# Kernel optimization log

Measured on AMD Instinct MI355X. Metric: run time of the kernel, lower is better.

Reference implementation:

```python
import jax, jax.numpy as jnp
import numpy as np

CH = 256
CH_HALF = CH // 2
HEADS = 2          # heads_half = max(1, 4 // 2)
WIN_R = (16, 4)
WIN_A = (4, 16)
EPS = 1e-5


def _rel_index(Wh, Ww):
    # Precomputed relative-position index, identical to RelPosBias.__init__
    coords = np.stack(np.meshgrid(np.arange(Wh), np.arange(Ww), indexing='ij'))
    coords = coords.reshape(2, -1)                      # [2, N]
    rel = coords[:, :, None] - coords[:, None, :]       # [2, N, N]
    rel = rel.transpose(1, 2, 0).copy()
    rel[..., 0] += Wh - 1
    rel[..., 1] += Ww - 1
    rel[..., 0] *= 2 * Ww - 1
    return jnp.asarray(rel.sum(-1))                     # [N, N] int


def _layernorm(x, g, b):
    m = jnp.mean(x, axis=-1, keepdims=True)
    v = jnp.mean((x - m) ** 2, axis=-1, keepdims=True)
    return (x - m) * jax.lax.rsqrt(v + EPS) * g + b


def _window_attn(xw, Wqkv, Wp, bp, table, window):
    # xw: [Bn, N, C]
    Bn, N, C = xw.shape
    d = C // HEADS
    qkv = (xw @ Wqkv).reshape(Bn, N, 3, HEADS, d).transpose(2, 0, 3, 1, 4)
    q, k, v = qkv[0], qkv[1], qkv[2]                    # [Bn, h, N, d]
    attn = jnp.einsum('bhnd,bhmd->bhnm', q, k) * (d ** -0.5)
    idx = _rel_index(*window)                           # [N, N]
    bias = table[idx.reshape(-1)].reshape(N, N, HEADS).transpose(2, 0, 1)
    attn = jax.nn.softmax(attn + bias[None], axis=-1)
    out = jnp.einsum('bhnm,bhmd->bhnd', attn, v)
    out = out.transpose(0, 2, 1, 3).reshape(Bn, N, C)
    return out @ Wp + bp


def _branch(x, window, Wqkv, Wp, bp, table):
    # x: [B, H, W, C]; window partition -> attn -> residual -> reverse
    B, H, W, C = x.shape
    Wh, Ww = window
    xw = x.reshape(B, H // Wh, Wh, W // Ww, Ww, C)
    xw = xw.transpose(0, 1, 3, 2, 4, 5).reshape(-1, Wh * Ww, C)
    xw = xw + _window_attn(xw, Wqkv, Wp, bp, table, window)
    x = xw.reshape(B, H // Wh, W // Ww, Wh, Ww, C)
    x = x.transpose(0, 1, 3, 2, 4, 5).reshape(B, H, W, C)
    return x


def setup_inputs() -> dict:
    key = jax.random.key(0)
    ks = jax.random.split(key, 16)
    N_R = (2 * WIN_R[0] - 1) * (2 * WIN_R[1] - 1)
    N_A = (2 * WIN_A[0] - 1) * (2 * WIN_A[1] - 1)
    s = lambda fan: (2.0 / fan) ** 0.5
    return {
        'x': jax.random.normal(ks[0], (1, CH, 256, 256), jnp.float32),
        'norm1_g': jnp.ones((CH,), jnp.float32),
        'norm1_b': jnp.zeros((CH,), jnp.float32),
        'qkv_r': jax.random.normal(ks[1], (CH_HALF, 3 * CH_HALF), jnp.float32) * s(CH_HALF),
        'proj_r_w': jax.random.normal(ks[2], (CH_HALF, CH_HALF), jnp.float32) * s(CH_HALF),
        'proj_r_b': jnp.zeros((CH_HALF,), jnp.float32),
        'table_r': jax.random.normal(ks[3], (N_R, HEADS), jnp.float32) * 0.02,
        'qkv_a': jax.random.normal(ks[4], (CH_HALF, 3 * CH_HALF), jnp.float32) * s(CH_HALF),
        'proj_a_w': jax.random.normal(ks[5], (CH_HALF, CH_HALF), jnp.float32) * s(CH_HALF),
        'proj_a_b': jnp.zeros((CH_HALF,), jnp.float32),
        'table_a': jax.random.normal(ks[6], (N_A, HEADS), jnp.float32) * 0.02,
        'norm2_g': jnp.ones((CH,), jnp.float32),
        'norm2_b': jnp.zeros((CH,), jnp.float32),
        'mlp_w1': jax.random.normal(ks[7], (CH, 4 * CH), jnp.float32) * s(CH),
        'mlp_b1': jnp.zeros((4 * CH,), jnp.float32),
        'mlp_w2': jax.random.normal(ks[8], (4 * CH, CH), jnp.float32) * s(4 * CH),
        'mlp_b2': jnp.zeros((CH,), jnp.float32),
    }


def reference(x, norm1_g, norm1_b, qkv_r, proj_r_w, proj_r_b, table_r,
              qkv_a, proj_a_w, proj_a_b, table_a, norm2_g, norm2_b,
              mlp_w1, mlp_b1, mlp_w2, mlp_b2):
    # x: [B, C, H, W]; H, W divisible by 16 -> pad is a no-op
    x = x.transpose(0, 2, 3, 1)                          # [B, H, W, C]
    idt = x
    xn = _layernorm(x, norm1_g, norm1_b)
    out_r = _branch(xn[..., :CH_HALF], WIN_R, qkv_r, proj_r_w, proj_r_b, table_r)
    out_a = _branch(xn[..., CH_HALF:], WIN_A, qkv_a, proj_a_w, proj_a_b, table_a)
    x = idt + jnp.concatenate([out_r, out_a], axis=-1)
    h = _layernorm(x, norm2_g, norm2_b)
    h = jax.nn.gelu(h @ mlp_w1 + mlp_b1, approximate=False) @ mlp_w2 + mlp_b2
    x = x + h
    return x.transpose(0, 3, 1, 2)                       # back to [B, C, H, W]
```

## Files before the change

kernel.cpp:

```cpp
#include <hip/hip_runtime.h>
#include <stdint.h>

typedef unsigned short ushort_t;
typedef __attribute__((ext_vector_type(8))) short short8;
typedef __attribute__((ext_vector_type(4))) float floatx4;
typedef __attribute__((ext_vector_type(16))) float floatx16;
typedef __attribute__((ext_vector_type(4))) unsigned int u32x4;

__device__ __forceinline__ float bf2f(ushort_t u) {
    union { unsigned int i; float f; } v; v.i = ((unsigned int)u) << 16; return v.f;
}
__device__ __forceinline__ ushort_t f2bf(float f) {
    union { float ff; unsigned int i; } v; v.ff = f;
    unsigned int x = v.i;
    return (ushort_t)((x + 0x7fffu + ((x >> 16) & 1u)) >> 16);
}
__device__ __forceinline__ float gelu_f(float v) {
    float u = v * (0.7978845608f + 0.0356774081f * v * v);
    float e = __expf(2.f * u);
    float th = 1.f - 2.f / (e + 1.f);
    return 0.5f * v * (1.f + th);
}
#define LDS_ROUNDTRIP_FENCE() __asm__ volatile("s_waitcnt lgkmcnt(0)" ::: "memory")

__global__ __launch_bounds__(256) void prep_k(
    const float* __restrict__ x, const float* __restrict__ n1g, const float* __restrict__ n1b,
    ushort_t* __restrict__ xn,
    const float* __restrict__ qkv_r, ushort_t* __restrict__ wqkvT_r,
    const float* __restrict__ qkv_a, ushort_t* __restrict__ wqkvT_a,
    const float* __restrict__ pr_w,  ushort_t* __restrict__ wpT_r,
    const float* __restrict__ pa_w,  ushort_t* __restrict__ wpT_a,
    const float* __restrict__ w1,    ushort_t* __restrict__ w1p,
    const float* __restrict__ w2,    ushort_t* __restrict__ w2p)
{
    __shared__ __align__(16) char pshm[33792];
    const int t = threadIdx.x;
    int b = blockIdx.x;
    if (b < 1024) {
        ushort_t* tile = (ushort_t*)pshm;
        const int p0 = b * 64;
        {
            const int pg = t & 15, cb = t >> 4;
            for (int it = 0; it < 16; ++it) {
                int c = cb + 16 * it;
                floatx4 v = *(const floatx4*)(x + (size_t)c * 65536 + p0 + pg * 4);
                #pragma unroll
                for (int k = 0; k < 4; ++k) tile[(pg * 4 + k) * 264 + c] = f2bf(v[k]);
            }
        }
        __syncthreads();
        const int pix = t >> 2, part = t & 3;
        float vals[64];
        float s = 0.f, ss = 0.f;
        #pragma unroll
        for (int k = 0; k < 64; ++k) {
            float v = bf2f(tile[pix * 264 + part * 64 + k]);
            vals[k] = v; s += v; ss += v * v;
        }
        s  += __shfl_xor(s, 1);  s  += __shfl_xor(s, 2);
        ss += __shfl_xor(ss, 1); ss += __shfl_xor(ss, 2);
        float mean = s * (1.f / 256.f);
        float rstd = rsqrtf(ss * (1.f / 256.f) - mean * mean + 1e-5f);
        size_t obase = (size_t)(p0 + pix) * 256 + part * 64;
        #pragma unroll
        for (int k8 = 0; k8 < 8; ++k8) {
            alignas(16) ushort_t o8[8];
            #pragma unroll
            for (int k = 0; k < 8; ++k) {
                int c = part * 64 + k8 * 8 + k;
                o8[k] = f2bf((vals[k8 * 8 + k] - mean) * rstd * n1g[c] + n1b[c]);
            }
            *(u32x4*)(xn + obase + k8 * 8) = *(const u32x4*)o8;
        }
        return;
    }
    b -= 1024;
    if (b < 512) {
        const float* src; ushort_t* dst; int R, C, bi;
        if (b < 192)      { src = qkv_r; dst = wqkvT_r; R = 128; C = 384; bi = b;       }
        else if (b < 384) { src = qkv_a; dst = wqkvT_a; R = 128; C = 384; bi = b - 192; }
        else if (b < 448) { src = pr_w;  dst = wpT_r;   R = 128; C = 128; bi = b - 384; }
        else              { src = pa_w;  dst = wpT_a;   R = 128; C = 128; bi = b - 448; }
        int nbx = C / 16;
        int c0 = (bi % nbx) * 16, r0 = (bi / nbx) * 16;
        float* ts = (float*)pshm;
        int tx = t & 15, ty = t >> 4;
        ts[ty * 17 + tx] = src[(size_t)(r0 + ty) * C + (c0 + tx)];
        __syncthreads();
        dst[(size_t)(c0 + ty) * R + (r0 + tx)] = f2bf(ts[tx * 17 + ty]);
        return;
    }
    b -= 512;
    float* s = (float*)pshm;
    if (b < 64) {
        const int ch = b & 15, k0 = (b >> 4) * 64;
        {
            int nn = t & 63, kr = t >> 6;
            for (int j = 0; j < 16; ++j) {
                int kk = j * 4 + kr;
                s[kk * 65 + nn] = w1[(size_t)(k0 + kk) * 1024 + ch * 64 + nn];
            }
        }
        __syncthreads();
        {
            int kk = t & 63, nr = t >> 6;
            for (int j = 0; j < 16; ++j) {
                int n2 = j * 4 + nr;
                w1p[(size_t)ch * 16896 + n2 * 264 + k0 + kk] = f2bf(s[kk * 65 + n2]);
            }
        }
        return;
    }
    b -= 64;
    {
        const int ch = b & 15, n0 = (b >> 4) * 64;
        {
            int nn = t & 63, kr = t >> 6;
            for (int j = 0; j < 16; ++j) {
                int kk = j * 4 + kr;
                s[kk * 65 + nn] = w2[(size_t)(ch * 64 + kk) * 256 + n0 + nn];
            }
        }
        __syncthreads();
        {
            int kk = t & 63, nr = t >> 6;
            for (int j = 0; j < 16; ++j) {
                int n2 = j * 4 + nr;
                w2p[(size_t)ch * 18432 + (n0 + n2) * 72 + kk] = f2bf(s[kk * 65 + n2]);
            }
        }
    }
}

__global__ __launch_bounds__(256, 2) void attn_k(
    const ushort_t* __restrict__ xn,
    const ushort_t* __restrict__ wqkvT_r, const ushort_t* __restrict__ wpT_r,
    const float* __restrict__ bp_r, const float* __restrict__ table_r,
    const ushort_t* __restrict__ wqkvT_a, const ushort_t* __restrict__ wpT_a,
    const float* __restrict__ bp_a, const float* __restrict__ table_a,
    ushort_t* __restrict__ bout)
{
    __shared__ __align__(16) char smem_raw[71680];
    ushort_t* xw_s = (ushort_t*)smem_raw;
    ushort_t* q_s  = (ushort_t*)(smem_raw + 17408);
    ushort_t* k_s  = (ushort_t*)(smem_raw + 35840);
    ushort_t* v_s  = (ushort_t*)(smem_raw + 53248);

    const int br  = blockIdx.y;
    const int wid = blockIdx.x;
    const int t = threadIdx.x;
    const int wv = t >> 6, lane = t & 63, l15 = lane & 15, quad = lane >> 4;

    const int WwLog = br ? 4 : 2;
    const int WhLog = br ? 2 : 4;
    const int nWxLog = 8 - WwLog;
    const int wx = wid & ((1 << nWxLog) - 1);
    const int wy = wid >> nWxLog;
    const int chOff = br ? 128 : 0;
    const int WwM1 = (1 << WwLog) - 1, WhM1 = (1 << WhLog) - 1;
    const int biasMul = 2 * (1 << WwLog) - 1;
    const ushort_t* wqkvT = br ? wqkvT_a : wqkvT_r;
    const ushort_t* wpT   = br ? wpT_a   : wpT_r;
    const float* bp    = br ? bp_a    : bp_r;
    const float* table = br ? table_a : table_r;

    auto tok2p = [&](int n) -> int {
        int i = n >> WwLog, j = n & WwM1;
        return ((wy << WhLog) + i) * 256 + (wx << WwLog) + j;
    };

    {
        int tok = t >> 2, seg = t & 3;
        const ushort_t* src = xn + (size_t)tok2p(tok) * 256 + chOff + seg * 32;
        ushort_t* dst = xw_s + tok * 136 + seg * 32;
        *(u32x4*)(dst)      = *(const u32x4*)(src);
        *(u32x4*)(dst + 8)  = *(const u32x4*)(src + 8);
        *(u32x4*)(dst + 16) = *(const u32x4*)(src + 16);
        *(u32x4*)(dst + 24) = *(const u32x4*)(src + 24);
    }
    __syncthreads();

    {
        short8 afrag[4];
        #pragma unroll
        for (int kt = 0; kt < 4; ++kt)
            afrag[kt] = *(const short8*)(xw_s + (16 * wv + l15) * 136 + kt * 32 + quad * 8);
        for (int nt = 0; nt < 24; ++nt) {
            floatx4 acc = {0.f, 0.f, 0.f, 0.f};
            const ushort_t* wb = wqkvT + (size_t)(nt * 16 + l15) * 128 + quad * 8;
            #pragma unroll
            for (int kt = 0; kt < 4; ++kt)
                acc = __builtin_amdgcn_mfma_f32_16x16x32_bf16(afrag[kt],
                        *(const short8*)(wb + kt * 32), acc, 0, 0, 0);
            int ncol = nt * 16 + l15;
            #pragma unroll
            for (int r = 0; r < 4; ++r) {
                int row = 16 * wv + quad * 4 + r;
                ushort_t val = f2bf(acc[r]);
                if (ncol < 128)      q_s[row * 136 + ncol] = val;
                else if (ncol < 256) k_s[row * 136 + (ncol - 128)] = val;
                else                 v_s[(ncol - 256) * 72 + row] = val;
            }
        }
    }
    __syncthreads();

    float pvals[2][4][4];
    #pragma unroll
    for (int head = 0; head < 2; ++head) {
        floatx4 sacc[4];
        #pragma unroll
        for (int nt = 0; nt < 4; ++nt) sacc[nt] = floatx4{0.f, 0.f, 0.f, 0.f};
        #pragma unroll
        for (int kt = 0; kt < 2; ++kt) {
            short8 aq = *(const short8*)(q_s + (16 * wv + l15) * 136 + head * 64 + kt * 32 + quad * 8);
            #pragma unroll
            for (int nt = 0; nt < 4; ++nt) {
                short8 bk = *(const short8*)(k_s + (nt * 16 + l15) * 136 + head * 64 + kt * 32 + quad * 8);
                sacc[nt] = __builtin_amdgcn_mfma_f32_16x16x32_bf16(aq, bk, sacc[nt], 0, 0, 0);
            }
        }
        #pragma unroll
        for (int r = 0; r < 4; ++r) {
            int qrow = 16 * wv + quad * 4 + r;
            int iq = qrow >> WwLog, jq = qrow & WwM1;
            float v[4], mx = -1e30f;
            #pragma unroll
            for (int nt = 0; nt < 4; ++nt) {
                int kcol = nt * 16 + l15;
                int ik = kcol >> WwLog, jk = kcol & WwM1;
                int idx = (iq - ik + WhM1) * biasMul + (jq - jk + WwM1);
                v[nt] = sacc[nt][r] * 0.125f + table[idx * 2 + head];
                mx = fmaxf(mx, v[nt]);
            }
            mx = fmaxf(mx, __shfl_xor(mx, 1)); mx = fmaxf(mx, __shfl_xor(mx, 2));
            mx = fmaxf(mx, __shfl_xor(mx, 4)); mx = fmaxf(mx, __shfl_xor(mx, 8));
            float e[4], sm = 0.f;
            #pragma unroll
            for (int nt = 0; nt < 4; ++nt) { e[nt] = __expf(v[nt] - mx); sm += e[nt]; }
            sm += __shfl_xor(sm, 1); sm += __shfl_xor(sm, 2);
            sm += __shfl_xor(sm, 4); sm += __shfl_xor(sm, 8);
            float inv = 1.f / sm;
            #pragma unroll
            for (int nt = 0; nt < 4; ++nt) pvals[head][nt][r] = e[nt] * inv;
        }
    }
    __syncthreads();

    {
        ushort_t* p_s = q_s;
        #pragma unroll
        for (int head = 0; head < 2; ++head)
            #pragma unroll
            for (int nt = 0; nt < 4; ++nt)
                #pragma unroll
                for (int r = 0; r < 4; ++r) {
                    int row = 16 * wv + quad * 4 + r;
                    p_s[(head * 64 + row) * 72 + nt * 16 + l15] = f2bf(pvals[head][nt][r]);
                }
    }
    LDS_ROUNDTRIP_FENCE();
    {
        const ushort_t* p_s = q_s;
        ushort_t* o_s = k_s;
        #pragma unroll
        for (int head = 0; head < 2; ++head) {
            short8 ap[2];
            #pragma unroll
            for (int kt = 0; kt < 2; ++kt)
                ap[kt] = *(const short8*)(p_s + (head * 64 + 16 * wv + l15) * 72 + kt * 32 + quad * 8);
            #pragma unroll
            for (int nt = 0; nt < 4; ++nt) {
                floatx4 acc = {0.f, 0.f, 0.f, 0.f};
                #pragma unroll
                for (int kt = 0; kt < 2; ++kt) {
                    short8 bv = *(const short8*)(v_s + (head * 64 + nt * 16 + l15) * 72 + kt * 32 + quad * 8);
                    acc = __builtin_amdgcn_mfma_f32_16x16x32_bf16(ap[kt], bv, acc, 0, 0, 0);
                }
                #pragma unroll
                for (int r = 0; r < 4; ++r)
                    o_s[(16 * wv + quad * 4 + r) * 136 + head * 64 + nt * 16 + l15] = f2bf(acc[r]);
            }
        }
    }
    __syncthreads();

    {
        const ushort_t* o_s = k_s;
        short8 ao[4];
        #pragma unroll
        for (int kt = 0; kt < 4; ++kt)
            ao[kt] = *(const short8*)(o_s + (16 * wv + l15) * 136 + kt * 32 + quad * 8);
        #pragma unroll
        for (int nt = 0; nt < 8; ++nt) {
            floatx4 acc = {0.f, 0.f, 0.f, 0.f};
            const ushort_t* wb = wpT + (size_t)(nt * 16 + l15) * 128 + quad * 8;
            #pragma unroll
            for (int kt = 0; kt < 4; ++kt)
                acc = __builtin_amdgcn_mfma_f32_16x16x32_bf16(ao[kt],
                        *(const short8*)(wb + kt * 32), acc, 0, 0, 0);
            int col = nt * 16 + l15;
            float bpv = bp[col];
            #pragma unroll
            for (int r = 0; r < 4; ++r) {
                int row = 16 * wv + quad * 4 + r;
                float res = acc[r] + bpv + bf2f(xw_s[row * 136 + col]);
                bout[(size_t)tok2p(row) * 256 + chOff + col] = f2bf(res);
            }
        }
    }
}

__global__ __launch_bounds__(256, 2) void mlp_k(
    const float* __restrict__ x,
    const ushort_t* __restrict__ bout,
    const float* __restrict__ g2, const float* __restrict__ b2,
    const ushort_t* __restrict__ w1p, const float* __restrict__ b1,
    const ushort_t* __restrict__ w2p, const float* __restrict__ bm2,
    float* __restrict__ out)
{
    __shared__ __align__(16) char smem_raw[79872];
    ushort_t* x2_s = (ushort_t*)smem_raw;
    ushort_t* wbuf = (ushort_t*)(smem_raw + 33792);
    ushort_t* hbuf = (ushort_t*)(smem_raw + 70656);
    ushort_t* xn_s = wbuf;
    ushort_t* ot_s = (ushort_t*)smem_raw;

    const int t = threadIdx.x;
    const int p0 = blockIdx.x * 64;
    const int wv = t >> 6, lane = t & 63, l31 = lane & 31, half = lane >> 5;

    {
        const int pg = t & 15, cb = t >> 4;
        for (int it = 0; it < 16; ++it) {
            int c = cb + 16 * it;
            floatx4 v = *(const floatx4*)(x + (size_t)c * 65536 + p0 + pg * 4);
            #pragma unroll
            for (int k = 0; k < 4; ++k) x2_s[(pg * 4 + k) * 264 + c] = f2bf(v[k]);
        }
    }
    __syncthreads();
    {
        const int row = t >> 2, part = t & 3;
        float vals[64];
        float s = 0.f, ss = 0.f;
        const ushort_t* bpr = bout + (size_t)(p0 + row) * 256 + part * 64;
        ushort_t* xpr = x2_s + row * 264 + part * 64;
        #pragma unroll
        for (int k8 = 0; k8 < 8; ++k8) {
            u32x4 bv = *(const u32x4*)(bpr + k8 * 8);
            u32x4 xv = *(const u32x4*)(xpr + k8 * 8);
            const ushort_t* pb = (const ushort_t*)&bv;
            const ushort_t* px = (const ushort_t*)&xv;
            #pragma unroll
            for (int k = 0; k < 8; ++k) {
                float v = bf2f(px[k]) + bf2f(pb[k]);
                vals[k8 * 8 + k] = v; s += v; ss += v * v;
            }
        }
        s  += __shfl_xor(s, 1);  s  += __shfl_xor(s, 2);
        ss += __shfl_xor(ss, 1); ss += __shfl_xor(ss, 2);
        float mean = s * (1.f / 256.f);
        float rstd = rsqrtf(ss * (1.f / 256.f) - mean * mean + 1e-5f);
        const float* g2p = g2 + part * 64;
        const float* b2p = b2 + part * 64;
        ushort_t* npr = xn_s + row * 264 + part * 64;
        #pragma unroll
        for (int k8 = 0; k8 < 8; ++k8) {
            alignas(16) ushort_t o8[8], n8[8];
            #pragma unroll
            for (int k = 0; k < 8; ++k) {
                float v = vals[k8 * 8 + k];
                o8[k] = f2bf(v);
                n8[k] = f2bf((v - mean) * rstd * g2p[k8 * 8 + k] + b2p[k8 * 8 + k]);
            }
            *(u32x4*)(xpr + k8 * 8) = *(const u32x4*)o8;
            *(u32x4*)(npr + k8 * 8) = *(const u32x4*)n8;
        }
    }
    __syncthreads();

    const int g1m = wv & 1, g1n = wv >> 1;
    const int g2m = wv & 1;
    const int g2nb = 128 * (wv >> 1);

    short8 afrag[16];
    #pragma unroll
    for (int ks = 0; ks < 16; ++ks)
        afrag[ks] = *(const short8*)(xn_s + (32 * g1m + l31) * 264 + ks * 16 + half * 8);

    u32x4* wb16 = (u32x4*)wbuf;
    u32x4 w1reg[9], w2reg[9];
    {
        const u32x4* s1 = (const u32x4*)w1p;
        #pragma unroll
        for (int j = 0; j < 8; ++j) w1reg[j] = s1[j * 256 + t];
        if (t < 64) w1reg[8] = s1[2048 + t];
    }
    __syncthreads();
    {
        #pragma unroll
        for (int j = 0; j < 8; ++j) wb16[j * 256 + t] = w1reg[j];
        if (t < 64) wb16[2048 + t] = w1reg[8];
    }
    __syncthreads();

    floatx16 oacc[4];
    #pragma unroll
    for (int nt = 0; nt < 4; ++nt)
        #pragma unroll
        for (int i = 0; i < 16; ++i) oacc[nt][i] = 0.f;

    for (int ch = 0; ch < 16; ++ch) {
        {
            const u32x4* s2 = (const u32x4*)(w2p + (size_t)ch * 18432);
            #pragma unroll
            for (int j = 0; j < 9; ++j) w2reg[j] = s2[j * 256 + t];
        }
        floatx16 ha, hb;
        #pragma unroll
        for (int i = 0; i < 16; ++i) { ha[i] = 0.f; hb[i] = 0.f; }
        #pragma unroll
        for (int ks = 0; ks < 16; ks += 2) {
            short8 bf0 = *(const short8*)(wbuf + (32 * g1n + l31) * 264 + ks * 16 + half * 8);
            short8 bf1 = *(const short8*)(wbuf + (32 * g1n + l31) * 264 + ks * 16 + 16 + half * 8);
            ha = __builtin_amdgcn_mfma_f32_32x32x16_bf16(afrag[ks], bf0, ha, 0, 0, 0);
            hb = __builtin_amdgcn_mfma_f32_32x32x16_bf16(afrag[ks + 1], bf1, hb, 0, 0, 0);
        }
        {
            float bb = b1[ch * 64 + 32 * g1n + l31];
            #pragma unroll
            for (int r = 0; r < 16; ++r) {
                int row = 32 * g1m + (r & 3) + 8 * (r >> 2) + 4 * half;
                float v = gelu_f(ha[r] + hb[r] + bb);
                hbuf[row * 72 + 32 * g1n + l31] = f2bf(v);
            }
        }
        __syncthreads();
        {
            #pragma unroll
            for (int j = 0; j < 9; ++j) wb16[j * 256 + t] = w2reg[j];
        }
        __syncthreads();
        if (ch < 15) {
            const u32x4* s1 = (const u32x4*)(w1p + (size_t)(ch + 1) * 16896);
            #pragma unroll
            for (int j = 0; j < 8; ++j) w1reg[j] = s1[j * 256 + t];
            if (t < 64) w1reg[8] = s1[2048 + t];
        }
        #pragma unroll
        for (int ks = 0; ks < 4; ++ks) {
            short8 haf = *(const short8*)(hbuf + (32 * g2m + l31) * 72 + ks * 16 + half * 8);
            #pragma unroll
            for (int nt = 0; nt < 4; ++nt) {
                short8 bfr = *(const short8*)(wbuf + (g2nb + 32 * nt + l31) * 72 + ks * 16 + half * 8);
                oacc[nt] = __builtin_amdgcn_mfma_f32_32x32x16_bf16(haf, bfr, oacc[nt], 0, 0, 0);
            }
        }
        __syncthreads();
        if (ch < 15) {
            #pragma unroll
            for (int j = 0; j < 8; ++j) wb16[j * 256 + t] = w1reg[j];
            if (t < 64) wb16[2048 + t] = w1reg[8];
        }
        __syncthreads();
    }

    #pragma unroll
    for (int nt = 0; nt < 4; ++nt) {
        int col = g2nb + 32 * nt + l31;
        float bb = bm2[col];
        #pragma unroll
        for (int r = 0; r < 16; ++r) {
            int row = 32 * g2m + (r & 3) + 8 * (r >> 2) + 4 * half;
            oacc[nt][r] += bb + bf2f(x2_s[row * 264 + col]);
        }
    }
    __syncthreads();
    #pragma unroll
    for (int nt = 0; nt < 4; ++nt) {
        int col = g2nb + 32 * nt + l31;
        #pragma unroll
        for (int r = 0; r < 16; ++r) {
            int row = 32 * g2m + (r & 3) + 8 * (r >> 2) + 4 * half;
            ot_s[col * 72 + row] = f2bf(oacc[nt][r]);
        }
    }
    __syncthreads();
    {
        for (int it = 0; it < 64; ++it) {
            int c = it * 4 + wv;
            out[(size_t)c * 65536 + p0 + lane] = bf2f(ot_s[c * 72 + lane]);
        }
    }
}

extern "C" void kernel_launch(void* const* d_in, const int* in_sizes, int n_in,
                              void* d_out, int out_size, void* d_ws, size_t ws_size,
                              hipStream_t stream) {
    (void)in_sizes; (void)n_in; (void)out_size; (void)ws_size;
    const float* x     = (const float*)d_in[0];
    const float* n1g   = (const float*)d_in[1];
    const float* n1b   = (const float*)d_in[2];
    const float* qkv_r = (const float*)d_in[3];
    const float* pr_w  = (const float*)d_in[4];
    const float* pr_b  = (const float*)d_in[5];
    const float* tab_r = (const float*)d_in[6];
    const float* qkv_a = (const float*)d_in[7];
    const float* pa_w  = (const float*)d_in[8];
    const float* pa_b  = (const float*)d_in[9];
    const float* tab_a = (const float*)d_in[10];
    const float* n2g   = (const float*)d_in[11];
    const float* n2b   = (const float*)d_in[12];
    const float* w1    = (const float*)d_in[13];
    const float* b1    = (const float*)d_in[14];
    const float* w2    = (const float*)d_in[15];
    const float* b2    = (const float*)d_in[16];

    char* ws = (char*)d_ws;
    ushort_t* wqkvT_r = (ushort_t*)(ws);
    ushort_t* wqkvT_a = (ushort_t*)(ws + 98304);
    ushort_t* wpT_r   = (ushort_t*)(ws + 196608);
    ushort_t* wpT_a   = (ushort_t*)(ws + 229376);
    ushort_t* w1p     = (ushort_t*)(ws + 262144);
    ushort_t* w2p     = (ushort_t*)(ws + 802816);
    ushort_t* bout    = (ushort_t*)(ws + 1392640);
    ushort_t* xn      = (ushort_t*)d_out;

    prep_k<<<1664, 256, 0, stream>>>(x, n1g, n1b, xn,
                                     qkv_r, wqkvT_r, qkv_a, wqkvT_a,
                                     pr_w, wpT_r, pa_w, wpT_a,
                                     w1, w1p, w2, w2p);
    attn_k<<<dim3(1024, 2), 256, 0, stream>>>(xn, wqkvT_r, wpT_r, pr_b, tab_r,
                                              wqkvT_a, wpT_a, pa_b, tab_a, bout);
    mlp_k<<<1024, 256, 0, stream>>>(x, bout, n2g, n2b, w1p, b1, w2p, b2, (float*)d_out);
}
```

Baseline: 428.4 us.

## Read MLP weight fragments directly from global and double-buffer hidden tiles

Result: slower. 502.4 us (+17.3%).

```diff
diff --git a/kernel.cpp b/kernel.cpp
--- a/kernel.cpp
+++ b/kernel.cpp
@@ -22,6 +22,7 @@
     return 0.5f * v * (1.f + th);
 }
 #define LDS_ROUNDTRIP_FENCE() __asm__ volatile("s_waitcnt lgkmcnt(0)" ::: "memory")
+#define BAR_SYNC_LDS() __asm__ volatile("s_waitcnt lgkmcnt(0)\n\ts_barrier" ::: "memory")
 
 __global__ __launch_bounds__(256) void prep_k(
     const float* __restrict__ x, const float* __restrict__ n1g, const float* __restrict__ n1b,
@@ -319,11 +320,11 @@
     const ushort_t* __restrict__ w2p, const float* __restrict__ bm2,
     float* __restrict__ out)
 {
-    __shared__ __align__(16) char smem_raw[79872];
+    __shared__ __align__(16) char smem_raw[67584];
     ushort_t* x2_s = (ushort_t*)smem_raw;
-    ushort_t* wbuf = (ushort_t*)(smem_raw + 33792);
-    ushort_t* hbuf = (ushort_t*)(smem_raw + 70656);
-    ushort_t* xn_s = wbuf;
+    ushort_t* xn_s = (ushort_t*)(smem_raw + 33792);
+    ushort_t* hb0  = (ushort_t*)(smem_raw + 33792);
+    ushort_t* hb1  = (ushort_t*)(smem_raw + 43008);
     ushort_t* ot_s = (ushort_t*)smem_raw;
 
     const int t = threadIdx.x;
@@ -388,21 +389,6 @@
     #pragma unroll
     for (int ks = 0; ks < 16; ++ks)
         afrag[ks] = *(const short8*)(xn_s + (32 * g1m + l31) * 264 + ks * 16 + half * 8);
-
-    u32x4* wb16 = (u32x4*)wbuf;
-    u32x4 w1reg[9], w2reg[9];
-    {
-        const u32x4* s1 = (const u32x4*)w1p;
-        #pragma unroll
-        for (int j = 0; j < 8; ++j) w1reg[j] = s1[j * 256 + t];
-        if (t < 64) w1reg[8] = s1[2048 + t];
-    }
-    __syncthreads();
-    {
-        #pragma unroll
-        for (int j = 0; j < 8; ++j) wb16[j * 256 + t] = w1reg[j];
-        if (t < 64) wb16[2048 + t] = w1reg[8];
-    }
     __syncthreads();
 
     floatx16 oacc[4];
@@ -411,60 +397,48 @@
         #pragma unroll
         for (int i = 0; i < 16; ++i) oacc[nt][i] = 0.f;
 
-    for (int ch = 0; ch < 16; ++ch) {
-        {
-            const u32x4* s2 = (const u32x4*)(w2p + (size_t)ch * 18432);
-            #pragma unroll
-            for (int j = 0; j < 9; ++j) w2reg[j] = s2[j * 256 + t];
-        }
+    const ushort_t* w1l = w1p + (size_t)(32 * g1n + l31) * 264 + half * 8;
+
+    auto gemm1 = [&](int ch, ushort_t* hbw) {
+        const ushort_t* w1c = w1l + (size_t)ch * 16896;
         floatx16 ha, hb;
         #pragma unroll
         for (int i = 0; i < 16; ++i) { ha[i] = 0.f; hb[i] = 0.f; }
         #pragma unroll
         for (int ks = 0; ks < 16; ks += 2) {
-            short8 bf0 = *(const short8*)(wbuf + (32 * g1n + l31) * 264 + ks * 16 + half * 8);
-            short8 bf1 = *(const short8*)(wbuf + (32 * g1n + l31) * 264 + ks * 16 + 16 + half * 8);
-            ha = __builtin_amdgcn_mfma_f32_32x32x16_bf16(afrag[ks], bf0, ha, 0, 0, 0);
+            short8 bf0 = *(const short8*)(w1c + ks * 16);
+            short8 bf1 = *(const short8*)(w1c + ks * 16 + 16);
+            ha = __builtin_amdgcn_mfma_f32_32x32x16_bf16(afrag[ks],     bf0, ha, 0, 0, 0);
             hb = __builtin_amdgcn_mfma_f32_32x32x16_bf16(afrag[ks + 1], bf1, hb, 0, 0, 0);
         }
-        {
-            float bb = b1[ch * 64 + 32 * g1n + l31];
-            #pragma unroll
-            for (int r = 0; r < 16; ++r) {
-                int row = 32 * g1m + (r & 3) + 8 * (r >> 2) + 4 * half;
-                float v = gelu_f(ha[r] + hb[r] + bb);
-                hbuf[row * 72 + 32 * g1n + l31] = f2bf(v);
-            }
-        }
-        __syncthreads();
-        {
-            #pragma unroll
-            for (int j = 0; j < 9; ++j) wb16[j * 256 + t] = w2reg[j];
-        }
-        __syncthreads();
-        if (ch < 15) {
-            const u32x4* s1 = (const u32x4*)(w1p + (size_t)(ch + 1) * 16896);
-            #pragma unroll
-            for (int j = 0; j < 8; ++j) w1reg[j] = s1[j * 256 + t];
-            if (t < 64) w1reg[8] = s1[2048 + t];
-        }
+        float bb = b1[ch * 64 + 32 * g1n + l31];
+        #pragma unroll
+        for (int r = 0; r < 16; ++r) {
+            int row = 32 * g1m + (r & 3) + 8 * (r >> 2) + 4 * half;
+            hbw[row * 72 + 32 * g1n + l31] = f2bf(gelu_f(ha[r] + hb[r] + bb));
+        }
+    };
+    auto gemm2 = [&](int ch, const ushort_t* hbr) {
         #pragma unroll
         for (int ks = 0; ks < 4; ++ks) {
-            short8 haf = *(const short8*)(hbuf + (32 * g2m + l31) * 72 + ks * 16 + half * 8);
+            short8 haf = *(const short8*)(hbr + (32 * g2m + l31) * 72 + ks * 16 + half * 8);
             #pragma unroll
             for (int nt = 0; nt < 4; ++nt) {
-                short8 bfr = *(const short8*)(wbuf + (g2nb + 32 * nt + l31) * 72 + ks * 16 + half * 8);
+                short8 bfr = *(const short8*)(w2p + (size_t)ch * 18432
+                                + (size_t)(g2nb + 32 * nt + l31) * 72 + ks * 16 + half * 8);
                 oacc[nt] = __builtin_amdgcn_mfma_f32_32x32x16_bf16(haf, bfr, oacc[nt], 0, 0, 0);
             }
         }
-        __syncthreads();
-        if (ch < 15) {
-            #pragma unroll
-            for (int j = 0; j < 8; ++j) wb16[j * 256 + t] = w1reg[j];
-            if (t < 64) wb16[2048 + t] = w1reg[8];
-        }
-        __syncthreads();
-    }
+    };
+
+    gemm1(0, hb0);
+    BAR_SYNC_LDS();
+    for (int ch = 0; ch < 15; ++ch) {
+        gemm1(ch + 1, (ch & 1) ? hb0 : hb1);
+        gemm2(ch,     (ch & 1) ? hb1 : hb0);
+        BAR_SYNC_LDS();
+    }
+    gemm2(15, hb1);
 
     #pragma unroll
     for (int nt = 0; nt < 4; ++nt) {
```

## Separate W1/W2 LDS buffers in MLP kernel, pad strides, recompute residual at output

Applied to the files above, without the earlier changes.

New measurement: 631.5 us. +47.4%, slower.

```diff
diff --git a/kernel.cpp b/kernel.cpp
--- a/kernel.cpp
+++ b/kernel.cpp
@@ -22,6 +22,12 @@
     return 0.5f * v * (1.f + th);
 }
 #define LDS_ROUNDTRIP_FENCE() __asm__ volatile("s_waitcnt lgkmcnt(0)" ::: "memory")
+#define BAR_SYNC_LDS() __asm__ volatile("s_waitcnt lgkmcnt(0)\n\ts_barrier" ::: "memory")
+
+#define W1_STRIDE 266
+#define W1_CHUNK  17024
+#define W2_STRIDE 74
+#define W2_CHUNK  18944
 
 __global__ __launch_bounds__(256) void prep_k(
     const float* __restrict__ x, const float* __restrict__ n1g, const float* __restrict__ n1b,
@@ -106,7 +112,7 @@
             int kk = t & 63, nr = t >> 6;
             for (int j = 0; j < 16; ++j) {
                 int n2 = j * 4 + nr;
-                w1p[(size_t)ch * 16896 + n2 * 264 + k0 + kk] = f2bf(s[kk * 65 + n2]);
+                w1p[(size_t)ch * W1_CHUNK + n2 * W1_STRIDE + k0 + kk] = f2bf(s[kk * 65 + n2]);
             }
         }
         return;
@@ -126,7 +132,7 @@
             int kk = t & 63, nr = t >> 6;
             for (int j = 0; j < 16; ++j) {
                 int n2 = j * 4 + nr;
-                w2p[(size_t)ch * 18432 + (n0 + n2) * 72 + kk] = f2bf(s[kk * 65 + n2]);
+                w2p[(size_t)ch * W2_CHUNK + (n0 + n2) * W2_STRIDE + kk] = f2bf(s[kk * 65 + n2]);
             }
         }
     }
@@ -319,11 +325,11 @@
     const ushort_t* __restrict__ w2p, const float* __restrict__ bm2,
     float* __restrict__ out)
 {
-    __shared__ __align__(16) char smem_raw[79872];
-    ushort_t* x2_s = (ushort_t*)smem_raw;
-    ushort_t* wbuf = (ushort_t*)(smem_raw + 33792);
-    ushort_t* hbuf = (ushort_t*)(smem_raw + 70656);
-    ushort_t* xn_s = wbuf;
+    __shared__ __align__(16) char smem_raw[81408];
+    ushort_t* w1b  = (ushort_t*)smem_raw;
+    ushort_t* w2b  = (ushort_t*)(smem_raw + 34048);
+    ushort_t* hbuf = (ushort_t*)(smem_raw + 71936);
+    ushort_t* tile = (ushort_t*)smem_raw;
     ushort_t* ot_s = (ushort_t*)smem_raw;
 
     const int t = threadIdx.x;
@@ -336,16 +342,16 @@
             int c = cb + 16 * it;
             floatx4 v = *(const floatx4*)(x + (size_t)c * 65536 + p0 + pg * 4);
             #pragma unroll
-            for (int k = 0; k < 4; ++k) x2_s[(pg * 4 + k) * 264 + c] = f2bf(v[k]);
-        }
-    }
-    __syncthreads();
+            for (int k = 0; k < 4; ++k) tile[(pg * 4 + k) * 264 + c] = f2bf(v[k]);
+        }
+    }
+    BAR_SYNC_LDS();
     {
         const int row = t >> 2, part = t & 3;
         float vals[64];
         float s = 0.f, ss = 0.f;
         const ushort_t* bpr = bout + (size_t)(p0 + row) * 256 + part * 64;
-        ushort_t* xpr = x2_s + row * 264 + part * 64;
+        ushort_t* xpr = tile + row * 264 + part * 64;
         #pragma unroll
         for (int k8 = 0; k8 < 8; ++k8) {
             u32x4 bv = *(const u32x4*)(bpr + k8 * 8);
@@ -364,21 +370,18 @@
         float rstd = rsqrtf(ss * (1.f / 256.f) - mean * mean + 1e-5f);
         const float* g2p = g2 + part * 64;
         const float* b2p = b2 + part * 64;
-        ushort_t* npr = xn_s + row * 264 + part * 64;
         #pragma unroll
         for (int k8 = 0; k8 < 8; ++k8) {
-            alignas(16) ushort_t o8[8], n8[8];
+            alignas(16) ushort_t n8[8];
             #pragma unroll
             for (int k = 0; k < 8; ++k) {
                 float v = vals[k8 * 8 + k];
-                o8[k] = f2bf(v);
                 n8[k] = f2bf((v - mean) * rstd * g2p[k8 * 8 + k] + b2p[k8 * 8 + k]);
             }
-            *(u32x4*)(xpr + k8 * 8) = *(const u32x4*)o8;
-            *(u32x4*)(npr + k8 * 8) = *(const u32x4*)n8;
-        }
-    }
-    __syncthreads();
+            *(u32x4*)(xpr + k8 * 8) = *(const u32x4*)n8;
+        }
+    }
+    BAR_SYNC_LDS();
 
     const int g1m = wv & 1, g1n = wv >> 1;
     const int g2m = wv & 1;
@@ -387,23 +390,31 @@
     short8 afrag[16];
     #pragma unroll
     for (int ks = 0; ks < 16; ++ks)
-        afrag[ks] = *(const short8*)(xn_s + (32 * g1m + l31) * 264 + ks * 16 + half * 8);
-
-    u32x4* wb16 = (u32x4*)wbuf;
-    u32x4 w1reg[9], w2reg[9];
+        afrag[ks] = *(const short8*)(tile + (32 * g1m + l31) * 264 + ks * 16 + half * 8);
+
+    u32x4* wb1 = (u32x4*)w1b;
+    u32x4* wb2 = (u32x4*)w2b;
+    u32x4 w1reg[9], w2reg[10];
     {
         const u32x4* s1 = (const u32x4*)w1p;
         #pragma unroll
         for (int j = 0; j < 8; ++j) w1reg[j] = s1[j * 256 + t];
-        if (t < 64) w1reg[8] = s1[2048 + t];
-    }
-    __syncthreads();
-    {
-        #pragma unroll
-        for (int j = 0; j < 8; ++j) wb16[j * 256 + t] = w1reg[j];
-        if (t < 64) wb16[2048 + t] = w1reg[8];
-    }
-    __syncthreads();
+        if (t < 80) w1reg[8] = s1[2048 + t];
+        const u32x4* s2 = (const u32x4*)w2p;
+        #pragma unroll
+        for (int j = 0; j < 9; ++j) w2reg[j] = s2[j * 256 + t];
+        if (t < 64) w2reg[9] = s2[2304 + t];
+    }
+    BAR_SYNC_LDS();
+    {
+        #pragma unroll
+        for (int j = 0; j < 8; ++j) wb1[j * 256 + t] = w1reg[j];
+        if (t < 80) wb1[2048 + t] = w1reg[8];
+        #pragma unroll
+        for (int j = 0; j < 9; ++j) wb2[j * 256 + t] = w2reg[j];
+        if (t < 64) wb2[2304 + t] = w2reg[9];
+    }
+    BAR_SYNC_LDS();
 
     floatx16 oacc[4];
     #pragma unroll
@@ -412,18 +423,19 @@
         for (int i = 0; i < 16; ++i) oacc[nt][i] = 0.f;
 
     for (int ch = 0; ch < 16; ++ch) {
-        {
-            const u32x4* s2 = (const u32x4*)(w2p + (size_t)ch * 18432);
-            #pragma unroll
-            for (int j = 0; j < 9; ++j) w2reg[j] = s2[j * 256 + t];
+        if (ch < 15) {
+            const u32x4* s1 = (const u32x4*)(w1p + (size_t)(ch + 1) * W1_CHUNK);
+            #pragma unroll
+            for (int j = 0; j < 8; ++j) w1reg[j] = s1[j * 256 + t];
+            if (t < 80) w1reg[8] = s1[2048 + t];
         }
         floatx16 ha, hb;
         #pragma unroll
         for (int i = 0; i < 16; ++i) { ha[i] = 0.f; hb[i] = 0.f; }
         #pragma unroll
         for (int ks = 0; ks < 16; ks += 2) {
-            short8 bf0 = *(const short8*)(wbuf + (32 * g1n + l31) * 264 + ks * 16 + half * 8);
-            short8 bf1 = *(const short8*)(wbuf + (32 * g1n + l31) * 264 + ks * 16 + 16 + half * 8);
+            short8 bf0 = *(const short8*)(w1b + (32 * g1n + l31) * W1_STRIDE + ks * 16 + half * 8);
+            short8 bf1 = *(const short8*)(w1b + (32 * g1n + l31) * W1_STRIDE + ks * 16 + 16 + half * 8);
             ha = __builtin_amdgcn_mfma_f32_32x32x16_bf16(afrag[ks], bf0, ha, 0, 0, 0);
             hb = __builtin_amdgcn_mfma_f32_32x32x16_bf16(afrag[ks + 1], bf1, hb, 0, 0, 0);
         }
@@ -433,37 +445,34 @@
             for (int r = 0; r < 16; ++r) {
                 int row = 32 * g1m + (r & 3) + 8 * (r >> 2) + 4 * half;
                 float v = gelu_f(ha[r] + hb[r] + bb);
-                hbuf[row * 72 + 32 * g1n + l31] = f2bf(v);
-            }
-        }
-        __syncthreads();
-        {
-            #pragma unroll
-            for (int j = 0; j < 9; ++j) wb16[j * 256 + t] = w2reg[j];
-        }
-        __syncthreads();
+                hbuf[row * W2_STRIDE + 32 * g1n + l31] = f2bf(v);
+            }
+        }
+        BAR_SYNC_LDS();
         if (ch < 15) {
-            const u32x4* s1 = (const u32x4*)(w1p + (size_t)(ch + 1) * 16896);
-            #pragma unroll
-            for (int j = 0; j < 8; ++j) w1reg[j] = s1[j * 256 + t];
-            if (t < 64) w1reg[8] = s1[2048 + t];
+            #pragma unroll
+            for (int j = 0; j < 8; ++j) wb1[j * 256 + t] = w1reg[j];
+            if (t < 80) wb1[2048 + t] = w1reg[8];
+            const u32x4* s2 = (const u32x4*)(w2p + (size_t)(ch + 1) * W2_CHUNK);
+            #pragma unroll
+            for (int j = 0; j < 9; ++j) w2reg[j] = s2[j * 256 + t];
+            if (t < 64) w2reg[9] = s2[2304 + t];
         }
         #pragma unroll
         for (int ks = 0; ks < 4; ++ks) {
-            short8 haf = *(const short8*)(hbuf + (32 * g2m + l31) * 72 + ks * 16 + half * 8);
+            short8 haf = *(const short8*)(hbuf + (32 * g2m + l31) * W2_STRIDE + ks * 16 + half * 8);
             #pragma unroll
             for (int nt = 0; nt < 4; ++nt) {
-                short8 bfr = *(const short8*)(wbuf + (g2nb + 32 * nt + l31) * 72 + ks * 16 + half * 8);
+                short8 bfr = *(const short8*)(w2b + (g2nb + 32 * nt + l31) * W2_STRIDE + ks * 16 + half * 8);
                 oacc[nt] = __builtin_amdgcn_mfma_f32_32x32x16_bf16(haf, bfr, oacc[nt], 0, 0, 0);
             }
         }
-        __syncthreads();
+        BAR_SYNC_LDS();
         if (ch < 15) {
             #pragma unroll
-            for (int j = 0; j < 8; ++j) wb16[j * 256 + t] = w1reg[j];
-            if (t < 64) wb16[2048 + t] = w1reg[8];
-        }
-        __syncthreads();
+            for (int j = 0; j < 9; ++j) wb2[j * 256 + t] = w2reg[j];
+            if (t < 64) wb2[2304 + t] = w2reg[9];
+        }
     }
 
     #pragma unroll
@@ -471,26 +480,28 @@
         int col = g2nb + 32 * nt + l31;
         float bb = bm2[col];
         #pragma unroll
-        for (int r = 0; r < 16; ++r) {
-            int row = 32 * g2m + (r & 3) + 8 * (r >> 2) + 4 * half;
-            oacc[nt][r] += bb + bf2f(x2_s[row * 264 + col]);
-        }
-    }
-    __syncthreads();
+        for (int r = 0; r < 16; ++r)
+            oacc[nt][r] += bb;
+    }
+    BAR_SYNC_LDS();
     #pragma unroll
     for (int nt = 0; nt < 4; ++nt) {
         int col = g2nb + 32 * nt + l31;
         #pragma unroll
         for (int r = 0; r < 16; ++r) {
             int row = 32 * g2m + (r & 3) + 8 * (r >> 2) + 4 * half;
-            ot_s[col * 72 + row] = f2bf(oacc[nt][r]);
-        }
-    }
-    __syncthreads();
+            ot_s[col * W2_STRIDE + row] = f2bf(oacc[nt][r]);
+        }
+    }
+    BAR_SYNC_LDS();
     {
         for (int it = 0; it < 64; ++it) {
             int c = it * 4 + wv;
-            out[(size_t)c * 65536 + p0 + lane] = bf2f(ot_s[c * 72 + lane]);
+            float accv = bf2f(ot_s[c * W2_STRIDE + lane]);
+            float xv   = x[(size_t)c * 65536 + p0 + lane];
+            float bo   = bf2f(bout[(size_t)(p0 + lane) * 256 + c]);
+            float x2v  = bf2f(f2bf(bf2f(f2bf(xv)) + bo));
+            out[(size_t)c * 65536 + p0 + lane] = accv + x2v;
         }
     }
 }
@@ -523,8 +534,8 @@
     ushort_t* wpT_r   = (ushort_t*)(ws + 196608);
     ushort_t* wpT_a   = (ushort_t*)(ws + 229376);
     ushort_t* w1p     = (ushort_t*)(ws + 262144);
-    ushort_t* w2p     = (ushort_t*)(ws + 802816);
-    ushort_t* bout    = (ushort_t*)(ws + 1392640);
+    ushort_t* w2p     = (ushort_t*)(ws + 806912);
+    ushort_t* bout    = (ushort_t*)(ws + 1413120);
     ushort_t* xn      = (ushort_t*)d_out;
 
     prep_k<<<1664, 256, 0, stream>>>(x, n1g, n1b, xn,
```
